# Kernel tuning notes

Measured on AMD Instinct MI355X. Metric: run time of the kernel, lower is better.

## Reference

```python
import math
import jax, jax.numpy as jnp
import numpy as np

B, S, D_IN, D_OUT = 8, 4096, 512, 512
CHUNK = 64
MAX_LR = 0.2        # config.max_memory_lr
MIN_DECAY = 0.5     # config.min_memory_decay
MAX_NORM = 30.0     # config.memory_max_norm
NORM_EPS = 1e-5     # config.norm_eps (used in normalize_for_delta)


def setup_inputs() -> dict:
    key = jax.random.key(0)
    ks = jax.random.split(key, 5)
    x = jax.random.normal(ks[0], (B, S, D_IN), dtype=jnp.float32)
    # M_init: xavier_uniform(gain=0.1) ~ small; use small normal
    M_init = jax.random.normal(ks[1], (D_OUT, D_IN), dtype=jnp.float32) * 0.02
    # hyperparam projections (Linear(d_in, 1)); torch init: zero weight, logit bias.
    # Use small random weights so the data-dependent path is exercised.
    eta_w = jax.random.normal(ks[2], (1, D_IN), dtype=jnp.float32) * 0.01
    eta_b = jnp.full((1,), math.log(0.08 / 0.92), dtype=jnp.float32)   # inv_sig(memory_lr_init)
    alpha_w = jax.random.normal(ks[3], (1, D_IN), dtype=jnp.float32) * 0.01
    alpha_b = jnp.full((1,), math.log(0.85 / 0.15), dtype=jnp.float32)  # inv_sig(memory_decay_init)
    gate_w = jax.random.normal(ks[4], (1, D_IN), dtype=jnp.float32) * 0.01
    gate_b = jnp.full((1,), 2.0, dtype=jnp.float32)
    return {"x": x, "M_init": M_init, "eta_w": eta_w, "eta_b": eta_b,
            "alpha_w": alpha_w, "alpha_b": alpha_b, "gate_w": gate_w, "gate_b": gate_b}


def _forward(x, M_init, eta_w, eta_b, alpha_w, alpha_b, gate_w, gate_b):
    n_chunks = S // CHUNK
    # [n_chunks, B, C, d_in] for scan over chunks
    xc = x.reshape(B, n_chunks, CHUNK, D_IN).transpose(1, 0, 2, 3)
    M0 = jnp.broadcast_to(M_init, (B, D_OUT, D_IN))

    def step(M, chunk):  # M: [B, d_out, d_in], chunk: [B, C, d_in]
        # per-chunk hyperparams (training mode: base logits = 0)
        eta_tok = jax.nn.sigmoid(chunk @ eta_w.T + eta_b) * MAX_LR            # [B,C,1]
        alpha_tok = MIN_DECAY + jax.nn.sigmoid(chunk @ alpha_w.T + alpha_b) * (1.0 - MIN_DECAY)
        eta = eta_tok.mean(axis=1, keepdims=True)    # [B,1,1]
        alpha = alpha_tok.mean(axis=1, keepdims=True)
        # retrieval: chunk @ M^T
        outputs = jnp.einsum('bcd,bod->bco', chunk, M)  # [B,C,d_out]
        # normalized keys (F.normalize: x / max(||x||, eps))
        kn = jnp.linalg.norm(chunk, axis=-1, keepdims=True)
        keys = chunk / jnp.maximum(kn, NORM_EPS)
        k_mean = keys.mean(axis=1)        # [B,d_in]
        v_target = outputs.mean(axis=1)   # [B,d_out]
        # delta rule rank-1 update
        Mk = jnp.einsum('bod,bd->bo', M, k_mean)
        error = v_target - Mk
        update = error[:, :, None] * k_mean[:, None, :]  # [B,d_out,d_in]
        # chunk_scale = min(C/chunk_size, 1) = 1 here
        M_new = alpha * M + eta * update
        gate = jax.nn.sigmoid(k_mean @ gate_w.T + gate_b)[:, :, None]  # [B,1,1]
        M_new = gate * M_new + (1.0 - gate) * M
        # frobenius-norm clamp
        M_norm = jnp.sqrt(jnp.sum(M_new * M_new, axis=(-2, -1), keepdims=True))
        scale = jnp.minimum(MAX_NORM / (M_norm + 1e-6), 1.0)
        return M_new * scale, outputs

    M_fin, outs = jax.lax.scan(step, M0, xc)  # outs: [n_chunks,B,C,d_out]
    out = outs.transpose(1, 0, 2, 3).reshape(B, S, D_OUT)
    return out, M_fin


def reference(x, M_init, eta_w, eta_b, alpha_w, alpha_b, gate_w, gate_b):
    return _forward(x, M_init, eta_w, eta_b, alpha_w, alpha_b, gate_w, gate_b)
```

## Files before the change

kernel.cpp:

```cpp
#include <hip/hip_runtime.h>
#include <math.h>

#define DIN  512
#define DOUT 512
#define CHK  64
#define NCH  64
#define NB   8
#define SEQ  4096

typedef short bh8_t __attribute__((ext_vector_type(8)));
typedef float f32x4 __attribute__((ext_vector_type(4)));

__device__ __forceinline__ float sigmoidf_(float z){ return 1.0f/(1.0f+__expf(-z)); }

__device__ __forceinline__ unsigned short f2bf(float f){
  unsigned u = __float_as_uint(f);
  unsigned r = (u + 0x7fffu + ((u>>16)&1u)) >> 16;
  return (unsigned short)r;
}
__device__ __forceinline__ void store_bf4(unsigned short* p, float4 v){
  uint2 u;
  u.x = (unsigned)f2bf(v.x) | ((unsigned)f2bf(v.y)<<16);
  u.y = (unsigned)f2bf(v.z) | ((unsigned)f2bf(v.w)<<16);
  *(uint2*)p = u;
}

__global__ __launch_bounds__(256) void k0_m0h(const float* __restrict__ M0, unsigned short* __restrict__ M0h){
  int idx = (blockIdx.x*256 + threadIdx.x)*4;
  float4 v = *(const float4*)(M0+idx);
  store_bf4(M0h+idx, v);
}

__global__ __launch_bounds__(256) void k1_stats(
    const float* __restrict__ x,
    const float* __restrict__ eta_w, const float* __restrict__ eta_b,
    const float* __restrict__ alpha_w, const float* __restrict__ alpha_b,
    const float* __restrict__ gate_w, const float* __restrict__ gate_b,
    float* __restrict__ KM, float* __restrict__ Dv, unsigned short* __restrict__ KMh,
    float* __restrict__ C1, float* __restrict__ C2, float* __restrict__ KM2, float* __restrict__ Q,
    unsigned short* __restrict__ xh)
{
  int j = blockIdx.x, b = blockIdx.y;
  const float* xc = x + ((size_t)b*SEQ + (size_t)j*CHK) * DIN;
  int tid = threadIdx.x;
  int wave = tid >> 6, lane = tid & 63;

  float km_acc[8], xb_acc[8];
#pragma unroll
  for (int k=0;k<8;k++){ km_acc[k]=0.f; xb_acc[k]=0.f; }
  float eta_sum = 0.f, alpha_sum = 0.f;
  float ew[8], aw[8];
#pragma unroll
  for (int k=0;k<8;k++){ ew[k]=eta_w[lane*8+k]; aw[k]=alpha_w[lane*8+k]; }

  for (int tt=0; tt<16; tt++){
    int t = wave*16 + tt;
    const float* xr = xc + (size_t)t*DIN + lane*8;
    float v[8];
#pragma unroll
    for (int k=0;k<8;k++) v[k]=xr[k];
    if (xh){
      uint4 hv;
      hv.x = (unsigned)f2bf(v[0]) | ((unsigned)f2bf(v[1])<<16);
      hv.y = (unsigned)f2bf(v[2]) | ((unsigned)f2bf(v[3])<<16);
      hv.z = (unsigned)f2bf(v[4]) | ((unsigned)f2bf(v[5])<<16);
      hv.w = (unsigned)f2bf(v[6]) | ((unsigned)f2bf(v[7])<<16);
      *(uint4*)&xh[((size_t)b*SEQ + (size_t)j*CHK + t)*DIN + lane*8] = hv;
    }
    float pe=0.f, pa=0.f, pn=0.f;
#pragma unroll
    for (int k=0;k<8;k++){ pe += v[k]*ew[k]; pa += v[k]*aw[k]; pn += v[k]*v[k]; }
#pragma unroll
    for (int off=32; off; off>>=1){
      pe += __shfl_xor(pe, off);
      pa += __shfl_xor(pa, off);
      pn += __shfl_xor(pn, off);
    }
    float inv = 1.0f / fmaxf(sqrtf(pn), 1e-5f);
    eta_sum   += sigmoidf_(pe + eta_b[0]);
    alpha_sum += sigmoidf_(pa + alpha_b[0]);
#pragma unroll
    for (int k=0;k<8;k++){ km_acc[k] += v[k]*inv; xb_acc[k] += v[k]; }
  }

  __shared__ float sKM[4][DIN];
  __shared__ float sXB[4][DIN];
  __shared__ float sEA[4][2];
  __shared__ float sred[4][2];
#pragma unroll
  for (int k=0;k<8;k++){ sKM[wave][lane*8+k]=km_acc[k]; sXB[wave][lane*8+k]=xb_acc[k]; }
  if (lane==0){ sEA[wave][0]=eta_sum; sEA[wave][1]=alpha_sum; }
  __syncthreads();

  float gpart=0.f, km2part=0.f;
  float kmv[2], dvv[2];
#pragma unroll
  for (int k=0;k<2;k++){
    int d = tid*2+k;
    float km = (sKM[0][d]+sKM[1][d]+sKM[2][d]+sKM[3][d]) * (1.0f/64.0f);
    float xb = (sXB[0][d]+sXB[1][d]+sXB[2][d]+sXB[3][d]) * (1.0f/64.0f);
    kmv[k]=km; dvv[k]=xb-km;
    gpart  += km * gate_w[d];
    km2part+= km * km;
  }
#pragma unroll
  for (int off=32; off; off>>=1){
    gpart   += __shfl_xor(gpart, off);
    km2part += __shfl_xor(km2part, off);
  }
  if (lane==0){ sred[wave][0]=gpart; sred[wave][1]=km2part; }
  __syncthreads();

  size_t base = ((size_t)b*NCH + j)*DIN;
#pragma unroll
  for (int k=0;k<2;k++){
    int d = tid*2+k;
    KM[base+d]=kmv[k];
    Dv[base+d]=dvv[k];
    KMh[base+d]=f2bf(kmv[k]);
  }
  if (tid==0){
    float gdot = sred[0][0]+sred[1][0]+sred[2][0]+sred[3][0];
    float km2  = sred[0][1]+sred[1][1]+sred[2][1]+sred[3][1];
    float etam = (sEA[0][0]+sEA[1][0]+sEA[2][0]+sEA[3][0]) * (1.0f/64.0f);
    float alpm = (sEA[0][1]+sEA[1][1]+sEA[2][1]+sEA[3][1]) * (1.0f/64.0f);
    float eta   = 0.2f * etam;
    float alpha = 0.5f + 0.5f * alpm;
    float gate  = sigmoidf_(gdot + gate_b[0]);
    float c1 = gate*alpha + 1.0f - gate;
    float c2 = gate*eta;
    C1[b*NCH+j]  = c1;
    C2[b*NCH+j]  = c2;
    KM2[b*NCH+j] = km2;
    Q[b*NCH+j]   = c2/c1;
  }
}

__global__ __launch_bounds__(256) void k2_g0h0(
    const float* __restrict__ KM, const float* __restrict__ Dv,
    const float* __restrict__ M0, float* __restrict__ G0, float* __restrict__ H0)
{
  int os = blockIdx.x, b = blockIdx.y;
  int o0 = os*16;
  __shared__ float sM0[16*DIN];
  int tid = threadIdx.x;
  {
    const float4* src = (const float4*)(M0 + (size_t)o0*DIN);
    float4* dst = (float4*)sM0;
#pragma unroll
    for (int v=0; v<8; v++) dst[v*256+tid] = src[v*256+tid];
  }
  __syncthreads();
  int o = tid>>4;
  int ks = tid&15;
  const float* m0r = sM0 + o*DIN + ks*32;
  for (int j=0;j<NCH;j++){
    size_t base = ((size_t)b*NCH+j)*DIN;
    const float4* kr = (const float4*)(KM + base + ks*32);
    const float4* dr = (const float4*)(Dv + base + ks*32);
    float ag=0.f, ah=0.f;
#pragma unroll
    for (int t=0;t<8;t++){
      float4 kv = kr[t], dv = dr[t];
      const float* mm = m0r + t*4;
      ah += mm[0]*kv.x + mm[1]*kv.y + mm[2]*kv.z + mm[3]*kv.w;
      ag += mm[0]*dv.x + mm[1]*dv.y + mm[2]*dv.z + mm[3]*dv.w;
    }
#pragma unroll
    for (int off=8; off; off>>=1){ ag += __shfl_xor(ag,off); ah += __shfl_xor(ah,off); }
    if (ks==0){ G0[base + o0 + o] = ag; H0[base + o0 + o] = ah; }
  }
}

__global__ __launch_bounds__(512) void k2b_gram(
    const float* __restrict__ KM, const float* __restrict__ Dv,
    const float* __restrict__ Q,
    float* __restrict__ GT, float* __restrict__ WT)
{
  int i = blockIdx.x, b = blockIdx.y;
  __shared__ float sKi[DIN];
  int tid = threadIdx.x;
  const float* kmi = KM + ((size_t)b*NCH+i)*DIN;
  for (int d=tid; d<DIN; d+=512) sKi[d]=kmi[d];
  __syncthreads();
  float qi = Q[b*NCH+i];
  int wave = tid>>6, lane = tid&63;
  for (int j=wave; j<NCH; j+=8){
    const float* dj = Dv + ((size_t)b*NCH+j)*DIN;
    const float* kj = KM + ((size_t)b*NCH+j)*DIN;
    float pd=0.f, pk=0.f;
#pragma unroll
    for (int k=0;k<8;k++){
      int d = lane + k*64;
      pd += sKi[d]*dj[d];
      pk += sKi[d]*kj[d];
    }
#pragma unroll
    for (int off=32; off; off>>=1){ pd += __shfl_xor(pd,off); pk += __shfl_xor(pk,off); }
    if (lane==0){
      GT[((size_t)b*NCH+j)*NCH + i] = qi*pd;
      WT[((size_t)b*NCH+j)*NCH + i] = qi*pk;
    }
  }
}

__global__ __launch_bounds__(64) void k3a_rec(
    const float* __restrict__ G0, const float* __restrict__ H0,
    const float* __restrict__ GT, const float* __restrict__ WT,
    const float* __restrict__ Q,
    float* __restrict__ AU, unsigned short* __restrict__ UQTh, float* __restrict__ DOTS)
{
  int dblk = blockIdx.x, b = blockIdx.y;
  int lane = threadIdx.x;
  int d = dblk*64 + lane;

  __shared__ float sMT[NCH*NCH];
  __shared__ float sWT[NCH*NCH];
  __shared__ float sq[NCH];

  const float4* gt4 = (const float4*)&GT[(size_t)b*NCH*NCH];
  const float4* wt4 = (const float4*)&WT[(size_t)b*NCH*NCH];
#pragma unroll
  for (int t=0;t<16;t++){
    int idx4 = t*64 + lane;
    int idx  = idx4*4;
    int j = idx>>6, i0 = idx&63;
    float4 g = gt4[idx4];
    float4 w = wt4[idx4];
    if (i0+0 >= j){ g.x=0.f; w.x=0.f; }
    if (i0+1 >= j){ g.y=0.f; w.y=0.f; }
    if (i0+2 >= j){ g.z=0.f; w.z=0.f; }
    if (i0+3 >= j){ g.w=0.f; w.w=0.f; }
    *(float4*)&sMT[idx] = g;
    *(float4*)&sWT[idx] = w;
  }
  sq[lane] = Q[b*NCH+lane];
  __syncthreads();

  float au[NCH];
  size_t gb = (size_t)b*NCH*DOUT + d;
#pragma unroll
  for (int j=0;j<NCH;j++) au[j] = G0[gb + (size_t)j*DOUT];

#pragma unroll
  for (int j=1;j<NCH;j++){
    float a = au[j];
    const f32x4* row = (const f32x4*)&sMT[j*64];
    int ng = (j+3)>>2;
#pragma unroll
    for (int g=0; g<ng; g++){
      f32x4 c = row[g];
      a += c[0]*au[g*4+0] + c[1]*au[g*4+1] + c[2]*au[g*4+2] + c[3]*au[g*4+3];
    }
    au[j] = a;
  }
#pragma unroll
  for (int j=0;j<NCH;j++) AU[gb + (size_t)j*DOUT] = au[j];

#pragma unroll
  for (int g=0; g<8; g++){
    uint4 hv;
    hv.x = (unsigned)f2bf(au[g*8+0]*sq[g*8+0]) | ((unsigned)f2bf(au[g*8+1]*sq[g*8+1])<<16);
    hv.y = (unsigned)f2bf(au[g*8+2]*sq[g*8+2]) | ((unsigned)f2bf(au[g*8+3]*sq[g*8+3])<<16);
    hv.z = (unsigned)f2bf(au[g*8+4]*sq[g*8+4]) | ((unsigned)f2bf(au[g*8+5]*sq[g*8+5])<<16);
    hv.w = (unsigned)f2bf(au[g*8+6]*sq[g*8+6]) | ((unsigned)f2bf(au[g*8+7]*sq[g*8+7])<<16);
    *(uint4*)&UQTh[((size_t)b*DOUT + d)*NCH + g*8] = hv;
  }

#pragma unroll
  for (int j=0;j<NCH;j++){
    float w = H0[gb + (size_t)j*DOUT];
    const f32x4* row = (const f32x4*)&sWT[j*64];
    int ng = (j+3)>>2;
#pragma unroll
    for (int g=0; g<ng; g++){
      f32x4 c = row[g];
      w += c[0]*au[g*4+0] + c[1]*au[g*4+1] + c[2]*au[g*4+2] + c[3]*au[g*4+3];
    }
    float s1 = au[j]*w, s2 = au[j]*au[j];
#pragma unroll
    for (int off=32; off; off>>=1){ s1+=__shfl_xor(s1,off); s2+=__shfl_xor(s2,off); }
    if (lane==0){
      DOTS[(((size_t)b*8+dblk)*NCH+j)*2+0] = s1;
      DOTS[(((size_t)b*8+dblk)*NCH+j)*2+1] = s2;
    }
  }
}

__global__ __launch_bounds__(256) void k3b_chain(
    const float* __restrict__ M0, const float* __restrict__ DOTS,
    const float* __restrict__ C1, const float* __restrict__ C2, const float* __restrict__ KM2,
    float* __restrict__ P)
{
  int b = blockIdx.x;
  int tid = threadIdx.x, wave = tid>>6, lane = tid&63;
  __shared__ float sF[4];
  __shared__ float suw[NCH], suu[NCH], sc1[NCH], sc2[NCH], skm2[NCH];

  float f0p = 0.f;
  const float4* m4 = (const float4*)M0;
  for (int i=tid; i<(DOUT*DIN)/4; i+=256){
    float4 v = m4[i];
    f0p += v.x*v.x + v.y*v.y + v.z*v.z + v.w*v.w;
  }
#pragma unroll
  for (int off=32; off; off>>=1) f0p += __shfl_xor(f0p, off);
  if (lane==0) sF[wave]=f0p;

  if (tid < NCH){
    float uw=0.f, uu=0.f;
#pragma unroll
    for (int k=0;k<8;k++){
      uw += DOTS[(((size_t)b*8+k)*NCH+tid)*2+0];
      uu += DOTS[(((size_t)b*8+k)*NCH+tid)*2+1];
    }
    suw[tid]=uw; suu[tid]=uu;
    sc1[tid]=C1[b*NCH+tid]; sc2[tid]=C2[b*NCH+tid]; skm2[tid]=KM2[b*NCH+tid];
  }
  __syncthreads();

  if (tid==0){
    float F = sF[0]+sF[1]+sF[2]+sF[3];
    float p = 1.f;
    P[b*65+0] = 1.f;
    for (int j=0;j<NCH;j++){
      float uw = suw[j], uu = suu[j];
      float c1 = sc1[j], c2 = sc2[j], km2 = skm2[j];
      uw *= p*p; uu *= p*p;
      float Fnew = c1*c1*F + 2.f*c1*c2*uw + c2*c2*uu*km2;
      float scale = fminf(30.0f/(sqrtf(Fnew)+1e-6f), 1.0f);
      F = scale*scale*Fnew;
      p = scale*c1*p;
      P[b*65+j+1] = p;
    }
  }
}

#define SSTRIDE 80
__global__ __launch_bounds__(256, 4) void k4s_s(
    const float* __restrict__ x, const unsigned short* __restrict__ xh,
    const unsigned short* __restrict__ KMh,
    unsigned short* __restrict__ Sh, int use_xh)
{
  int rb = blockIdx.x, b = blockIdx.y;
  int R0 = rb*128;
  int tid = threadIdx.x;
  int lane = tid&63, w = tid>>6, m = lane&15, q = lane>>4;
  int wr = w>>1, wc = w&1;

  __shared__ unsigned short As[128*SSTRIDE];
  __shared__ unsigned short Bs[64*SSTRIDE];

  f32x4 acc[4][2];
  f32x4 z = {0.f,0.f,0.f,0.f};
#pragma unroll
  for (int mi=0;mi<4;mi++)
#pragma unroll
    for (int nf=0;nf<2;nf++) acc[mi][nf]=z;

  uint4 pB[2], pA[4];
  float4 xa[8];
#pragma unroll
  for (int v=0;v<2;v++){
    int idx=v*256+tid; int il=idx>>3, cc=idx&7;
    pB[v] = *(const uint4*)&KMh[((size_t)b*NCH+il)*DIN + 0 + cc*8];
  }
  if (use_xh){
#pragma unroll
    for (int v=0;v<4;v++){
      int idx=v*256+tid; int row=idx>>3, cc=idx&7;
      pA[v] = *(const uint4*)&xh[((size_t)b*SEQ + R0 + row)*DIN + 0 + cc*8];
    }
  } else {
#pragma unroll
    for (int v=0;v<8;v++){
      int idx=v*256+tid; int row=idx>>4, cc=idx&15;
      xa[v] = *(const float4*)(x + ((size_t)b*SEQ + R0 + row)*DIN + 0 + cc*4);
    }
  }

  for (int k0=0;k0<DIN;k0+=64){
    __syncthreads();
#pragma unroll
    for (int v=0;v<2;v++){
      int idx=v*256+tid; int il=idx>>3, cc=idx&7;
      *(uint4*)&Bs[il*SSTRIDE + cc*8] = pB[v];
    }
    if (use_xh){
#pragma unroll
      for (int v=0;v<4;v++){
        int idx=v*256+tid; int row=idx>>3, cc=idx&7;
        *(uint4*)&As[row*SSTRIDE + cc*8] = pA[v];
      }
    } else {
#pragma unroll
      for (int v=0;v<8;v++){
        int idx=v*256+tid; int row=idx>>4, cc=idx&15;
        store_bf4(&As[row*SSTRIDE + cc*4], xa[v]);
      }
    }
    int kn = k0 + 64;
    if (kn < DIN){
#pragma unroll
      for (int v=0;v<2;v++){
        int idx=v*256+tid; int il=idx>>3, cc=idx&7;
        pB[v] = *(const uint4*)&KMh[((size_t)b*NCH+il)*DIN + kn + cc*8];
      }
      if (use_xh){
#pragma unroll
        for (int v=0;v<4;v++){
          int idx=v*256+tid; int row=idx>>3, cc=idx&7;
          pA[v] = *(const uint4*)&xh[((size_t)b*SEQ + R0 + row)*DIN + kn + cc*8];
        }
      } else {
#pragma unroll
        for (int v=0;v<8;v++){
          int idx=v*256+tid; int row=idx>>4, cc=idx&15;
          xa[v] = *(const float4*)(x + ((size_t)b*SEQ + R0 + row)*DIN + kn + cc*4);
        }
      }
    }
    __syncthreads();
#pragma unroll
    for (int kk=0;kk<2;kk++){
#pragma unroll
      for (int mi=0;mi<4;mi++){
        bh8_t af = *(bh8_t*)&As[(wr*64+mi*16+m)*SSTRIDE + kk*32 + q*8];
#pragma unroll
        for (int nf=0;nf<2;nf++){
          bh8_t bf_ = *(bh8_t*)&Bs[(wc*32+nf*16+m)*SSTRIDE + kk*32 + q*8];
          acc[mi][nf] = __builtin_amdgcn_mfma_f32_16x16x32_bf16(af, bf_, acc[mi][nf], 0,0,0);
        }
      }
    }
  }

  __syncthreads();
  unsigned short* tb = As + w*16*40;
#pragma unroll
  for (int mi=0; mi<4; mi++){
#pragma unroll
    for (int nf=0;nf<2;nf++)
#pragma unroll
      for (int r=0;r<4;r++)
        tb[(q*4+r)*40 + nf*16 + m] = f2bf(acc[mi][nf][r]);
    int row = lane>>2, c8 = lane&3;
    uint4 vv = *(uint4*)&tb[row*40 + c8*8];
    *(uint4*)&Sh[((size_t)b*SEQ + R0 + wr*64 + mi*16 + row)*NCH + wc*32 + c8*8] = vv;
  }
}

#define ASTRIDE 80
__global__ __launch_bounds__(512, 4) void k4_out(
    const float* __restrict__ x, const unsigned short* __restrict__ xh,
    const unsigned short* __restrict__ M0h,
    const unsigned short* __restrict__ Sh, const unsigned short* __restrict__ UQTh,
    const float* __restrict__ P, float* __restrict__ out, int use_xh)
{
  int n = blockIdx.x;
  int xcd = n & 7, local = n >> 3;
  int work = xcd*64 + local;
  int ot = work & 3, rb = (work>>2) & 15, b = work >> 6;

  int tid = threadIdx.x;
  int lane = tid&63, w = tid>>6, m = lane&15, q = lane>>4;
  int wr = w>>1, wc = w&1;
  int O0 = ot*128;
  int R0 = rb*256;

  __shared__ __align__(16) char pool[(256+128)*ASTRIDE*2];
  unsigned short* As = (unsigned short*)pool;
  unsigned short* Bs = (unsigned short*)pool + 256*ASTRIDE;
  float* ep = (float*)pool;

  f32x4 acc[4][4];
  f32x4 z = {0.f,0.f,0.f,0.f};
#pragma unroll
  for (int mi=0;mi<4;mi++)
#pragma unroll
    for (int nf=0;nf<4;nf++) acc[mi][nf]=z;

#pragma unroll
  for (int v=0; v<4; v++){
    int idx = v*512 + tid;
    int row = idx>>3, cc = idx&7;
    int j = (R0 + row)>>6;
    uint4 sv = *(const uint4*)&Sh[((size_t)b*SEQ + R0 + row)*NCH + cc*8];
    int i0 = cc*8;
    unsigned m0 = (i0+0 < j) ? ((i0+1 < j)?0xFFFFFFFFu:0x0000FFFFu) : 0u;
    unsigned m1 = (i0+2 < j) ? ((i0+3 < j)?0xFFFFFFFFu:0x0000FFFFu) : 0u;
    unsigned m2 = (i0+4 < j) ? ((i0+5 < j)?0xFFFFFFFFu:0x0000FFFFu) : 0u;
    unsigned m3 = (i0+6 < j) ? ((i0+7 < j)?0xFFFFFFFFu:0x0000FFFFu) : 0u;
    sv.x&=m0; sv.y&=m1; sv.z&=m2; sv.w&=m3;
    *(uint4*)&As[row*ASTRIDE + cc*8] = sv;
  }
#pragma unroll
  for (int v=0; v<2; v++){
    int idx = v*512 + tid;
    int ol = idx>>3, cc = idx&7;
    *(uint4*)&Bs[ol*ASTRIDE + cc*8] = *(const uint4*)&UQTh[((size_t)b*DOUT + O0+ol)*NCH + cc*8];
  }

  uint4 pB[2], pA[4];
  float4 xa[8];
#pragma unroll
  for (int v=0;v<2;v++){
    int idx=v*512+tid; int ol=idx>>3, cc=idx&7;
    pB[v] = *(const uint4*)&M0h[(size_t)(O0+ol)*DIN + 0 + cc*8];
  }
  if (use_xh){
#pragma unroll
    for (int v=0;v<4;v++){
      int idx=v*512+tid; int row=idx>>3, cc=idx&7;
      pA[v] = *(const uint4*)&xh[((size_t)b*SEQ + R0 + row)*DIN + 0 + cc*8];
    }
  } else {
#pragma unroll
    for (int v=0;v<8;v++){
      int idx=v*512+tid; int row=idx>>4, cc=idx&15;
      xa[v] = *(const float4*)(x + ((size_t)b*SEQ + R0 + row)*DIN + 0 + cc*4);
    }
  }

  __syncthreads();
#pragma unroll
  for (int kk=0;kk<2;kk++){
#pragma unroll
    for (int mi=0;mi<4;mi++){
      bh8_t af = *(bh8_t*)&As[(wr*64+mi*16+m)*ASTRIDE + kk*32 + q*8];
#pragma unroll
      for (int nf=0;nf<4;nf++){
        bh8_t bf_ = *(bh8_t*)&Bs[(wc*64+nf*16+m)*ASTRIDE + kk*32 + q*8];
        acc[mi][nf] = __builtin_amdgcn_mfma_f32_16x16x32_bf16(af, bf_, acc[mi][nf], 0,0,0);
      }
    }
  }

  for (int k0=0;k0<DIN;k0+=64){
    __syncthreads();
#pragma unroll
    for (int v=0;v<2;v++){
      int idx=v*512+tid; int ol=idx>>3, cc=idx&7;
      *(uint4*)&Bs[ol*ASTRIDE + cc*8] = pB[v];
    }
    if (use_xh){
#pragma unroll
      for (int v=0;v<4;v++){
        int idx=v*512+tid; int row=idx>>3, cc=idx&7;
        *(uint4*)&As[row*ASTRIDE + cc*8] = pA[v];
      }
    } else {
#pragma unroll
      for (int v=0;v<8;v++){
        int idx=v*512+tid; int row=idx>>4, cc=idx&15;
        store_bf4(&As[row*ASTRIDE + cc*4], xa[v]);
      }
    }
    int kn = k0 + 64;
    if (kn < DIN){
#pragma unroll
      for (int v=0;v<2;v++){
        int idx=v*512+tid; int ol=idx>>3, cc=idx&7;
        pB[v] = *(const uint4*)&M0h[(size_t)(O0+ol)*DIN + kn + cc*8];
      }
      if (use_xh){
#pragma unroll
        for (int v=0;v<4;v++){
          int idx=v*512+tid; int row=idx>>3, cc=idx&7;
          pA[v] = *(const uint4*)&xh[((size_t)b*SEQ + R0 + row)*DIN + kn + cc*8];
        }
      } else {
#pragma unroll
        for (int v=0;v<8;v++){
          int idx=v*512+tid; int row=idx>>4, cc=idx&15;
          xa[v] = *(const float4*)(x + ((size_t)b*SEQ + R0 + row)*DIN + kn + cc*4);
        }
      }
    }
    __syncthreads();
#pragma unroll
    for (int kk=0;kk<2;kk++){
#pragma unroll
      for (int mi=0;mi<4;mi++){
        bh8_t af = *(bh8_t*)&As[(wr*64+mi*16+m)*ASTRIDE + kk*32 + q*8];
#pragma unroll
        for (int nf=0;nf<4;nf++){
          bh8_t bf_ = *(bh8_t*)&Bs[(wc*64+nf*16+m)*ASTRIDE + kk*32 + q*8];
          acc[mi][nf] = __builtin_amdgcn_mfma_f32_16x16x32_bf16(af, bf_, acc[mi][nf], 0,0,0);
        }
      }
    }
  }

  __syncthreads();
  float p = P[b*65 + rb*4 + wr];
  float* epw = ep + w*(16*68);
#pragma unroll
  for (int mi=0; mi<4; mi++){
#pragma unroll
    for (int nf=0;nf<4;nf++)
#pragma unroll
      for (int r=0;r<4;r++)
        epw[(q*4+r)*68 + nf*16 + m] = p*acc[mi][nf][r];
#pragma unroll
    for (int v=0;v<4;v++){
      int idx = v*64 + lane;
      int row = idx>>4, c4 = idx&15;
      f32x4 vv = *(f32x4*)&epw[row*68 + c4*4];
      f32x4* pdst = (f32x4*)&out[((size_t)b*SEQ + R0 + wr*64 + mi*16 + row)*DOUT + O0 + wc*64 + c4*4];
      __builtin_nontemporal_store(vv, pdst);
    }
  }
}

__global__ __launch_bounds__(256) void k5_mfin(
    const float* __restrict__ M0, const float* __restrict__ KM,
    const float* __restrict__ AU, const float* __restrict__ P, const float* __restrict__ Q,
    float* __restrict__ Mout)
{
  int ob = blockIdx.x, b = blockIdx.y;
  int tid = threadIdx.x;
  __shared__ float uo[64][8];
  for (int idx=tid; idx<512; idx+=256){
    int i = idx>>3, oo = idx&7;
    uo[i][oo] = Q[b*NCH+i] * AU[((size_t)b*NCH+i)*DOUT + ob*8+oo];
  }
  __syncthreads();
  float p64 = P[b*65+NCH];
  float acc[2][8];
#pragma unroll
  for (int h=0;h<2;h++)
#pragma unroll
    for (int oo=0;oo<8;oo++) acc[h][oo]=0.f;
  int d0 = tid, d1 = tid+256;
  for (int i=0;i<64;i++){
    float k0 = KM[((size_t)b*NCH+i)*DIN + d0];
    float k1 = KM[((size_t)b*NCH+i)*DIN + d1];
#pragma unroll
    for (int oo=0;oo<8;oo++){
      float u = uo[i][oo];
      acc[0][oo] += u*k0;
      acc[1][oo] += u*k1;
    }
  }
#pragma unroll
  for (int oo=0;oo<8;oo++){
    int o = ob*8+oo;
    Mout[((size_t)b*DOUT + o)*DIN + d0] = p64*(M0[(size_t)o*DIN+d0] + acc[0][oo]);
    Mout[((size_t)b*DOUT + o)*DIN + d1] = p64*(M0[(size_t)o*DIN+d1] + acc[1][oo]);
  }
}

extern "C" void kernel_launch(void* const* d_in, const int* in_sizes, int n_in,
                              void* d_out, int out_size, void* d_ws, size_t ws_size,
                              hipStream_t stream) {
  const float* x       = (const float*)d_in[0];
  const float* M0      = (const float*)d_in[1];
  const float* eta_w   = (const float*)d_in[2];
  const float* eta_b   = (const float*)d_in[3];
  const float* alpha_w = (const float*)d_in[4];
  const float* alpha_b = (const float*)d_in[5];
  const float* gate_w  = (const float*)d_in[6];
  const float* gate_b  = (const float*)d_in[7];
  float* out = (float*)d_out;

  float* ws = (float*)d_ws;
  float* KM   = ws;
  float* Dv   = KM   + 262144;
  float* G0   = Dv   + 262144;
  float* H0   = G0   + 262144;
  float* AU   = H0   + 262144;
  float* GT   = AU   + 262144;
  float* WT   = GT   + 32768;
  float* C1   = WT   + 32768;
  float* C2   = C1   + 512;
  float* KM2  = C2   + 512;
  float* Q    = KM2  + 512;
  float* P    = Q    + 512;
  float* DOTS = P    + 1024;
  unsigned short* M0h  = (unsigned short*)(DOTS + 8192);
  unsigned short* KMh  = M0h  + 262144;
  unsigned short* Sh   = KMh  + 262144;
  unsigned short* UQTh = Sh   + 2097152;
  unsigned short* xh   = UQTh + 262144;

  size_t base_bytes = (size_t)((char*)xh - (char*)d_ws);
  size_t need_xh = base_bytes + (size_t)16777216*2;
  int use_xh = (ws_size >= need_xh) ? 1 : 0;
  unsigned short* xh_arg = use_xh ? xh : (unsigned short*)0;

  k0_m0h<<<dim3(256), 256, 0, stream>>>(M0, M0h);
  k1_stats<<<dim3(NCH, NB), 256, 0, stream>>>(x, eta_w, eta_b, alpha_w, alpha_b,
                                              gate_w, gate_b, KM, Dv, KMh, C1, C2, KM2, Q, xh_arg);
  k2_g0h0<<<dim3(32, NB), 256, 0, stream>>>(KM, Dv, M0, G0, H0);
  k2b_gram<<<dim3(NCH, NB), 512, 0, stream>>>(KM, Dv, Q, GT, WT);
  k4s_s<<<dim3(SEQ/128, NB), 256, 0, stream>>>(x, xh, KMh, Sh, use_xh);
  k3a_rec<<<dim3(8, NB), 64, 0, stream>>>(G0, H0, GT, WT, Q, AU, UQTh, DOTS);
  k3b_chain<<<dim3(NB), 256, 0, stream>>>(M0, DOTS, C1, C2, KM2, P);
  k4_out<<<dim3(512), 512, 0, stream>>>(x, xh, M0h, Sh, UQTh, P, out, use_xh);
  k5_mfin<<<dim3(64, NB), 256, 0, stream>>>(M0, KM, AU, P, Q, out + (size_t)NB*SEQ*DOUT);
}
```

Baseline: 525.0 us.

## Parallelize G0/H0 kernel over chunks instead of output-row slices

Restructures k2_g0h0 so each block handles one (chunk, batch, half) with 256 threads each computing one output row's dot products against the chunk's Dv and KM vectors held in shared memory. The old version used 256 blocks that each looped sequentially over all 64 chunks. The new grid has 1024 blocks and no serial chunk loop, which exposes more parallelism. In exchange, M0 rows are read per thread straight from global memory with a row-strided, uncoalesced float4 pattern, and M0 is re-read by every chunk block.

New measurement: 479.9 us. -8.6%, faster.

```diff
diff --git a/kernel.cpp b/kernel.cpp
--- a/kernel.cpp
+++ b/kernel.cpp
@@ -140,36 +140,21 @@
     const float* __restrict__ KM, const float* __restrict__ Dv,
     const float* __restrict__ M0, float* __restrict__ G0, float* __restrict__ H0)
 {
-  int os = blockIdx.x, b = blockIdx.y;
-  int o0 = os*16;
-  __shared__ float sM0[16*DIN];
+  int j = blockIdx.x, b = blockIdx.y, half = blockIdx.z;
+  __shared__ float sD[DIN], sK[DIN];
   int tid = threadIdx.x;
-  {
-    const float4* src = (const float4*)(M0 + (size_t)o0*DIN);
-    float4* dst = (float4*)sM0;
-#pragma unroll
-    for (int v=0; v<8; v++) dst[v*256+tid] = src[v*256+tid];
-  }
-  __syncthreads();
-  int o = tid>>4;
-  int ks = tid&15;
-  const float* m0r = sM0 + o*DIN + ks*32;
-  for (int j=0;j<NCH;j++){
-    size_t base = ((size_t)b*NCH+j)*DIN;
-    const float4* kr = (const float4*)(KM + base + ks*32);
-    const float4* dr = (const float4*)(Dv + base + ks*32);
-    float ag=0.f, ah=0.f;
-#pragma unroll
-    for (int t=0;t<8;t++){
-      float4 kv = kr[t], dv = dr[t];
-      const float* mm = m0r + t*4;
-      ah += mm[0]*kv.x + mm[1]*kv.y + mm[2]*kv.z + mm[3]*kv.w;
-      ag += mm[0]*dv.x + mm[1]*dv.y + mm[2]*dv.z + mm[3]*dv.w;
-    }
-#pragma unroll
-    for (int off=8; off; off>>=1){ ag += __shfl_xor(ag,off); ah += __shfl_xor(ah,off); }
-    if (ks==0){ G0[base + o0 + o] = ag; H0[base + o0 + o] = ah; }
-  }
+  size_t base = ((size_t)b*NCH+j)*DIN;
+  for (int d=tid; d<DIN; d+=256){ sD[d]=Dv[base+d]; sK[d]=KM[base+d]; }
+  __syncthreads();
+  int o = half*256 + tid;
+  const float* mr = M0 + (size_t)o*DIN;
+  float ag=0.f, ah=0.f;
+  for (int d=0; d<DIN; d+=4){
+    float4 m = *(const float4*)(mr+d);
+    ag += m.x*sD[d] + m.y*sD[d+1] + m.z*sD[d+2] + m.w*sD[d+3];
+    ah += m.x*sK[d] + m.y*sK[d+1] + m.z*sK[d+2] + m.w*sK[d+3];
+  }
+  G0[base+o]=ag; H0[base+o]=ah;
 }
 
 __global__ __launch_bounds__(512) void k2b_gram(
@@ -692,7 +677,7 @@
   k0_m0h<<<dim3(256), 256, 0, stream>>>(M0, M0h);
   k1_stats<<<dim3(NCH, NB), 256, 0, stream>>>(x, eta_w, eta_b, alpha_w, alpha_b,
                                               gate_w, gate_b, KM, Dv, KMh, C1, C2, KM2, Q, xh_arg);
-  k2_g0h0<<<dim3(32, NB), 256, 0, stream>>>(KM, Dv, M0, G0, H0);
+  k2_g0h0<<<dim3(NCH, NB, 2), 256, 0, stream>>>(KM, Dv, M0, G0, H0);
   k2b_gram<<<dim3(NCH, NB), 512, 0, stream>>>(KM, Dv, Q, GT, WT);
   k4s_s<<<dim3(SEQ/128, NB), 256, 0, stream>>>(x, xh, KMh, Sh, use_xh);
   k3a_rec<<<dim3(8, NB), 64, 0, stream>>>(G0, H0, GT, WT, Q, AU, UQTh, DOTS);
```
